# Kernel tuning notes

Hardware: AMD Instinct MI355X
Metric: run time of the kernel (lower is better)

Reference implementation:

```python
import jax, jax.numpy as jnp
import numpy as np

B, NA, NR, D, CUTOFF = 128, 32, 300, 128, 8.0


def _normalize(v, eps=1e-8):
    return v / jnp.maximum(jnp.linalg.norm(v, axis=-1, keepdims=True), eps)


def setup_inputs() -> dict:
    rng = np.random.default_rng(0)
    pl = rng.uniform(0.0, 24.0, (B, NA, 3)).astype(np.float32)
    pr = rng.uniform(0.0, 24.0, (B, NR, 3)).astype(np.float32)
    el_list, er_list = [], []
    for g in range(B):  # bipartite radius graph per complex (preprocessing)
        d2 = ((pl[g][:, None, :] - pr[g][None, :, :]) ** 2).sum(-1)
        li, ri = np.nonzero(d2 < CUTOFF * CUTOFF)
        el_list.append(li + g * NA)
        er_list.append(ri + g * NR)
    el = np.concatenate(el_list).astype(np.int32)
    er = np.concatenate(er_list).astype(np.int32)

    L, Dq = 2, D // 4
    def lin(k, shape, fan_in):
        return (rng.standard_normal(shape).astype(np.float32) / np.sqrt(fan_in))
    inp = {
        'ligand_repr': jnp.asarray(rng.standard_normal((B * NA, D)).astype(np.float32)),
        'ligand_vec_input': jnp.asarray(rng.standard_normal((B * NA, 3)).astype(np.float32)),
        'pos_ligand': jnp.asarray(pl.reshape(-1, 3)),
        'residue_repr': jnp.asarray(rng.standard_normal((B * NR, D)).astype(np.float32)),
        'pos_residue': jnp.asarray(pr.reshape(-1, 3)),
        'batch_ligand': jnp.asarray(np.repeat(np.arange(B), NA).astype(np.int32)),
        'batch_residue': jnp.asarray(np.repeat(np.arange(B), NR).astype(np.int32)),
        'edge_ligand_idx': jnp.asarray(el),
        'edge_residue_idx': jnp.asarray(er),
        # per-layer params stacked on leading L axis (stored [in,out])
        'Win1': jnp.asarray(lin(0, (L, D, D), D)),   'bin1': jnp.zeros((L, D), jnp.float32),
        'Win2': jnp.asarray(lin(0, (L, D, D), D)),   'bin2': jnp.zeros((L, D), jnp.float32),
        'Ws1a': jnp.asarray(lin(0, (L, 3, Dq), 3)),  'bs1a': jnp.zeros((L, Dq), jnp.float32),
        'Ws1b': jnp.asarray(lin(0, (L, Dq, 1), Dq)), 'bs1b': jnp.zeros((L, 1), jnp.float32),
        'Ws2a': jnp.asarray(lin(0, (L, 3, Dq), 3)),  'bs2a': jnp.zeros((L, Dq), jnp.float32),
        'Ws2b': jnp.asarray(lin(0, (L, Dq, 1), Dq)), 'bs2b': jnp.zeros((L, 1), jnp.float32),
        'Wl1': jnp.asarray(lin(0, (D, D), D)),       'bl1': jnp.zeros((D,), jnp.float32),
        'Wl2': jnp.asarray(lin(0, (D, 1), D)),       'bl2': jnp.zeros((1,), jnp.float32),
    }
    return inp


def reference(ligand_repr, ligand_vec_input, pos_ligand, residue_repr, pos_residue,
              batch_ligand, batch_residue, edge_ligand_idx, edge_residue_idx,
              Win1, bin1, Win2, bin2, Ws1a, bs1a, Ws1b, bs1b,
              Ws2a, bs2a, Ws2b, bs2b, Wl1, bl1, Wl2, bl2):
    Nl = pos_ligand.shape[0]
    L = Win1.shape[0]
    # residue local frames from consecutive backbone directions
    u = _normalize(pos_residue[1:] - pos_residue[:-1])      # [Nr-1, 3]
    start, end = u[1:], u[:-1]
    diff = _normalize(end - start)
    cross = _normalize(jnp.cross(end, start))
    vertical = _normalize(jnp.cross(diff, cross))
    frame = jnp.stack([diff, cross, vertical], axis=1)       # [Nr-2, 3, 3]
    residue_frame = jnp.concatenate([frame[:1], frame, frame[-1:]], axis=0)  # [Nr, 3, 3]

    edge_diff = _normalize(pos_ligand[edge_ligand_idx] - pos_residue[edge_residue_idx])  # [E, 3]
    # proj[e, j] = sum_i edge_diff[e, i] * frame[er[e], i, j]
    proj = jnp.einsum('ei,eij->ej', edge_diff, residue_frame[edge_residue_idx])  # [E, 3]
    h_sum = ligand_repr[edge_ligand_idx] + residue_repr[edge_residue_idx]        # [E, D]

    ligand_vec = jnp.zeros((Nl, 3, ligand_repr.shape[1]), ligand_repr.dtype)
    for l in range(L):
        h = jax.nn.silu(h_sum @ Win1[l] + bin1[l]) @ Win2[l] + bin2[l]           # [E, D]
        perm = h[:, :, None] * proj[:, None, :]                                  # [E, D, 3]
        w01 = (jax.nn.silu(perm @ Ws1a[l] + bs1a[l]) @ Ws1b[l] + bs1b[l]).squeeze(-1) + perm[..., 0]
        w02 = (jax.nn.silu(perm @ Ws2a[l] + bs2a[l]) @ Ws2b[l] + bs2b[l]).squeeze(-1) + perm[..., 0]
        lv_exp = ligand_vec[edge_ligand_idx] * w01[:, None, :] + edge_diff[:, :, None] * w02[:, None, :]
        ligand_vec = ligand_vec + jax.ops.segment_sum(lv_exp, edge_ligand_idx, num_segments=Nl)

    out = (jax.nn.relu(ligand_vec @ Wl1 + bl1) @ Wl2 + bl2).squeeze(-1) + ligand_vec_input  # [Nl, 3]
    return out
```

## Files before the change

### kernel.cpp

```cpp
#include <hip/hip_runtime.h>
#include <hip/hip_bf16.h>
#include <math.h>

typedef short bf16x8 __attribute__((ext_vector_type(8)));
typedef float f32x4 __attribute__((ext_vector_type(4)));

union BU8 { uint4 u; __hip_bfloat16 h[8]; ushort s[8]; };

__device__ __forceinline__ float3 f3sub(float3 a, float3 b){ return make_float3(a.x-b.x, a.y-b.y, a.z-b.z); }
__device__ __forceinline__ float3 f3nrm(float3 v){
  float n = sqrtf(v.x*v.x + v.y*v.y + v.z*v.z);
  float inv = 1.0f / fmaxf(n, 1e-8f);
  return make_float3(v.x*inv, v.y*inv, v.z*inv);
}
__device__ __forceinline__ float3 f3cross(float3 a, float3 b){
  return make_float3(a.y*b.z - a.z*b.y, a.z*b.x - a.x*b.z, a.x*b.y - a.y*b.x);
}
__device__ __forceinline__ float silu_f(float x){
  float ex = __expf(-x);
  return x * __builtin_amdgcn_rcpf(1.0f + ex);
}
__device__ __forceinline__ uint packbf2(float a, float b){
  ushort ua = __bfloat16_as_ushort(__float2bfloat16(a));
  ushort ub = __bfloat16_as_ushort(__float2bfloat16(b));
  return (uint)ua | ((uint)ub << 16);
}

__global__ void frames_kernel(const float* __restrict__ pos, float* __restrict__ frames, int Nr){
  int n = blockIdx.x*blockDim.x + threadIdx.x;
  if (n >= Nr) return;
  int k = n - 1;
  if (k < 0) k = 0;
  int kmax = Nr - 3;
  if (k > kmax) k = kmax;
  float3 p0 = make_float3(pos[3*k+0], pos[3*k+1], pos[3*k+2]);
  float3 p1 = make_float3(pos[3*k+3], pos[3*k+4], pos[3*k+5]);
  float3 p2 = make_float3(pos[3*k+6], pos[3*k+7], pos[3*k+8]);
  float3 u0 = f3nrm(f3sub(p1,p0));
  float3 u1 = f3nrm(f3sub(p2,p1));
  float3 dif = f3nrm(f3sub(u0,u1));
  float3 cr  = f3nrm(f3cross(u0,u1));
  float3 vt  = f3nrm(f3cross(dif,cr));
  float* o = frames + (size_t)n*9;
  o[0]=dif.x; o[1]=dif.y; o[2]=dif.z;
  o[3]=cr.x;  o[4]=cr.y;  o[5]=cr.z;
  o[6]=vt.x;  o[7]=vt.y;  o[8]=vt.z;
}

__global__ void edgepre_kernel(const float* __restrict__ posl, const float* __restrict__ posr,
    const int* __restrict__ el, const int* __restrict__ er, const float* __restrict__ frames,
    float* __restrict__ ediff, float* __restrict__ proj, int E){
  int e = blockIdx.x*blockDim.x + threadIdx.x;
  if (e >= E) return;
  int a = el[e], r = er[e];
  float3 pa = make_float3(posl[3*a+0], posl[3*a+1], posl[3*a+2]);
  float3 pr = make_float3(posr[3*r+0], posr[3*r+1], posr[3*r+2]);
  float3 ed = f3nrm(f3sub(pa,pr));
  const float* F = frames + (size_t)r*9;
  float px = ed.x*F[0] + ed.y*F[3] + ed.z*F[6];
  float py = ed.x*F[1] + ed.y*F[4] + ed.z*F[7];
  float pz = ed.x*F[2] + ed.y*F[5] + ed.z*F[8];
  ediff[3*e+0]=ed.x; ediff[3*e+1]=ed.y; ediff[3*e+2]=ed.z;
  proj[3*e+0]=px; proj[3*e+1]=py; proj[3*e+2]=pz;
}

__global__ void wprep_kernel(const float* __restrict__ W, __hip_bfloat16* __restrict__ Wt, int total){
  int idx = blockIdx.x*blockDim.x + threadIdx.x;
  if (idx >= total) return;
  int l = idx >> 14, rem = idx & 16383, n = rem >> 7, k = rem & 127;
  Wt[idx] = __float2bfloat16(W[(l<<14) + (k<<7) + n]);
}

__global__ __launch_bounds__(256) void pre_gemm_mfma(
    const float* __restrict__ lig, const float* __restrict__ res,
    const __hip_bfloat16* __restrict__ W1t,
    __hip_bfloat16* __restrict__ ligLb, __hip_bfloat16* __restrict__ resLb,
    int nBlkLig, int Nl, int Nr)
{
  __shared__ __hip_bfloat16 sA[64][136];
  __shared__ __hip_bfloat16 sB[128][136];
  int b = blockIdx.x;
  int layer = blockIdx.y;
  const __hip_bfloat16* Wt = W1t + (size_t)layer*16384;
  const float* X; __hip_bfloat16* O; int row0, rows;
  if (b < nBlkLig){ X = lig; O = ligLb + (size_t)layer*Nl*128; row0 = b*64;           rows = Nl; }
  else            { X = res; O = resLb + (size_t)layer*Nr*128; row0 = (b-nBlkLig)*64; rows = Nr; }
  int tid = threadIdx.x;

  {
    int n = tid >> 1, c0 = (tid & 1) * 64;
    const ushort* src = (const ushort*)Wt + n*128 + c0;
    ushort* dst = (ushort*)&sB[n][0] + c0;
    #pragma unroll
    for (int i = 0; i < 64; i += 8) *(uint4*)(dst + i) = *(const uint4*)(src + i);
  }
  {
    int r = tid >> 2, p = tid & 3, cb = p*32;
    int row = row0 + r; if (row >= rows) row = rows - 1;
    const float* src = X + (size_t)row*128 + cb;
    ushort* dst = (ushort*)&sA[r][0] + cb;
    #pragma unroll
    for (int i = 0; i < 32; i += 8){
      float4 v0 = *(const float4*)(src + i);
      float4 v1 = *(const float4*)(src + i + 4);
      BU8 o;
      o.h[0]=__float2bfloat16(v0.x); o.h[1]=__float2bfloat16(v0.y);
      o.h[2]=__float2bfloat16(v0.z); o.h[3]=__float2bfloat16(v0.w);
      o.h[4]=__float2bfloat16(v1.x); o.h[5]=__float2bfloat16(v1.y);
      o.h[6]=__float2bfloat16(v1.z); o.h[7]=__float2bfloat16(v1.w);
      *(uint4*)(dst + i) = o.u;
    }
  }
  __syncthreads();

  int w = tid >> 6, l = tid & 63;
  int lrow = l & 15, lko = (l >> 4) * 8;
  f32x4 acc[4][2];
  for (int mt=0; mt<4; ++mt)
    for (int nt=0; nt<2; ++nt)
      acc[mt][nt] = (f32x4){0.f,0.f,0.f,0.f};

  #pragma unroll
  for (int kc = 0; kc < 128; kc += 32){
    bf16x8 af[4], bfr[2];
    #pragma unroll
    for (int mt=0; mt<4; ++mt)
      af[mt] = *(const bf16x8*)((const ushort*)&sA[0][0] + (mt*16+lrow)*136 + kc + lko);
    #pragma unroll
    for (int nt=0; nt<2; ++nt)
      bfr[nt] = *(const bf16x8*)((const ushort*)&sB[0][0] + (w*32+nt*16+lrow)*136 + kc + lko);
    #pragma unroll
    for (int mt=0; mt<4; ++mt){
      #pragma unroll
      for (int nt=0; nt<2; ++nt)
        acc[mt][nt] = __builtin_amdgcn_mfma_f32_16x16x32_bf16(af[mt], bfr[nt], acc[mt][nt], 0, 0, 0);
    }
  }

  int orow = (l >> 4) * 4;
  #pragma unroll
  for (int mt=0; mt<4; ++mt){
    #pragma unroll
    for (int nt=0; nt<2; ++nt){
      int n = w*32 + nt*16 + (l & 15);
      #pragma unroll
      for (int j=0; j<4; ++j){
        int row = row0 + mt*16 + orow + j;
        if (row < rows) O[(size_t)row*128 + n] = __float2bfloat16(acc[mt][nt][j]);
      }
    }
  }
}

__global__ __launch_bounds__(256) void h_gemm2_mfma(
    const __hip_bfloat16* __restrict__ ligLbB, const __hip_bfloat16* __restrict__ resLbB,
    const int* __restrict__ el, const int* __restrict__ er,
    const float* __restrict__ b1B, const __hip_bfloat16* __restrict__ W2tB,
    const float* __restrict__ b2B,
    __hip_bfloat16* __restrict__ houtB, int E, int Nl, int Nr)
{
  __shared__ __hip_bfloat16 sA[64][136];
  __shared__ __hip_bfloat16 sB[128][136];
  int tid = threadIdx.x;
  int e0 = blockIdx.x * 64;
  int layer = blockIdx.y;
  const __hip_bfloat16* ligLb = ligLbB + (size_t)layer*Nl*128;
  const __hip_bfloat16* resLb = resLbB + (size_t)layer*Nr*128;
  const float* b1 = b1B + layer*128;
  const __hip_bfloat16* W2t = W2tB + (size_t)layer*16384;
  const float* b2 = b2B + layer*128;
  __hip_bfloat16* hout = houtB + (size_t)layer*E*128;

  {
    int n = tid >> 1, c0 = (tid & 1) * 64;
    const ushort* src = (const ushort*)W2t + n*128 + c0;
    ushort* dst = (ushort*)&sB[n][0] + c0;
    #pragma unroll
    for (int i = 0; i < 64; i += 8) *(uint4*)(dst + i) = *(const uint4*)(src + i);
  }
  {
    int r = tid >> 2, p = tid & 3, cb = p*32;
    int e = e0 + r; if (e >= E) e = E - 1;
    const ushort* la = (const ushort*)ligLb + (size_t)el[e]*128 + cb;
    const ushort* ra = (const ushort*)resLb + (size_t)er[e]*128 + cb;
    ushort* dst = (ushort*)&sA[r][0] + cb;
    #pragma unroll
    for (int i = 0; i < 32; i += 8){
      BU8 A, B, O;
      A.u = *(const uint4*)(la + i);
      B.u = *(const uint4*)(ra + i);
      float4 bb0 = *(const float4*)(b1 + cb + i);
      float4 bbx = *(const float4*)(b1 + cb + i + 4);
      float bbs[8] = {bb0.x,bb0.y,bb0.z,bb0.w,bbx.x,bbx.y,bbx.z,bbx.w};
      #pragma unroll
      for (int j=0; j<8; ++j){
        float x = __bfloat162float(A.h[j]) + __bfloat162float(B.h[j]) + bbs[j];
        O.h[j] = __float2bfloat16(silu_f(x));
      }
      *(uint4*)(dst + i) = O.u;
    }
  }
  __syncthreads();

  int w = tid >> 6, l = tid & 63;
  int lrow = l & 15, lko = (l >> 4) * 8;
  f32x4 acc[4][2];
  for (int mt=0; mt<4; ++mt)
    for (int nt=0; nt<2; ++nt)
      acc[mt][nt] = (f32x4){0.f,0.f,0.f,0.f};

  #pragma unroll
  for (int kc = 0; kc < 128; kc += 32){
    bf16x8 af[4], bfr[2];
    #pragma unroll
    for (int mt=0; mt<4; ++mt)
      af[mt] = *(const bf16x8*)((const ushort*)&sA[0][0] + (mt*16+lrow)*136 + kc + lko);
    #pragma unroll
    for (int nt=0; nt<2; ++nt)
      bfr[nt] = *(const bf16x8*)((const ushort*)&sB[0][0] + (w*32+nt*16+lrow)*136 + kc + lko);
    #pragma unroll
    for (int mt=0; mt<4; ++mt){
      #pragma unroll
      for (int nt=0; nt<2; ++nt)
        acc[mt][nt] = __builtin_amdgcn_mfma_f32_16x16x32_bf16(af[mt], bfr[nt], acc[mt][nt], 0, 0, 0);
    }
  }

  int orow = (l >> 4) * 4;
  #pragma unroll
  for (int mt=0; mt<4; ++mt){
    #pragma unroll
    for (int nt=0; nt<2; ++nt){
      int n = w*32 + nt*16 + (l & 15);
      float bb = b2[n];
      #pragma unroll
      for (int j=0; j<4; ++j){
        int e = e0 + mt*16 + orow + j;
        if (e < E) hout[(size_t)e*128 + n] = __float2bfloat16(acc[mt][nt][j] + bb);
      }
    }
  }
}

#define SEPB 16
__global__ __launch_bounds__(256) void spline_kernel(
    __hip_bfloat16* __restrict__ hbufB, const float* __restrict__ proj,
    const float* __restrict__ Ws1a, const float* __restrict__ bs1a,
    const float* __restrict__ Ws1b, const float* __restrict__ bs1b,
    const float* __restrict__ Ws2a, const float* __restrict__ bs2a,
    const float* __restrict__ Ws2b, const float* __restrict__ bs2b,
    __hip_bfloat16* __restrict__ w02B, int E)
{
  int layer = blockIdx.y;
  const float* Wa1 = Ws1a + layer*96;  const float* ba1 = bs1a + layer*32;
  const float* Wb1 = Ws1b + layer*32;  const float* bb1 = bs1b + layer;
  const float* Wa2 = Ws2a + layer*96;  const float* ba2 = bs2a + layer*32;
  const float* Wb2 = Ws2b + layer*32;  const float* bb2 = bs2b + layer;
  __hip_bfloat16* hb  = hbufB + (size_t)layer*E*128;
  __hip_bfloat16* w2o = w02B  + (size_t)layer*E*128;

  __shared__ float sA[2][SEPB][36];
  __shared__ float sNF[SEPB][2][16];
  __shared__ ushort sH[SEPB][128];
  __shared__ uint  sCo[SEPB][52];
  __shared__ float sMin[SEPB], sMax[SEPB];
  __shared__ float sH0[SEPB], sDv[SEPB], sInvD[SEPB], sP0[SEPB];

  int tid = threadIdx.x;
  int eb0 = blockIdx.x * SEPB;

  {
    int et = tid >> 4, sg = tid & 15;
    int e = eb0 + et; if (e >= E) e = E-1;
    uint4 raw = *(const uint4*)((const ushort*)hb + (size_t)e*128 + sg*8);
    *(uint4*)&sH[et][sg*8] = raw;
    uint us[4] = {raw.x, raw.y, raw.z, raw.w};
    float mn = 1e30f, mx = -1e30f;
    #pragma unroll
    for (int i=0;i<4;i++){
      float lo = __uint_as_float(us[i]<<16);
      float hi = __uint_as_float(us[i]&0xFFFF0000u);
      mn = fminf(mn, fminf(lo,hi)); mx = fmaxf(mx, fmaxf(lo,hi));
    }
    #pragma unroll
    for (int o=8;o>0;o>>=1){ mn=fminf(mn,__shfl_xor(mn,o)); mx=fmaxf(mx,__shfl_xor(mx,o)); }
    if (sg==0){ sMin[et]=mn; sMax[et]=mx; }
  }
  __syncthreads();

  for (int t=tid; t<2*SEPB*32; t+=256){
    int et = t>>6, rem = t&63, br = rem>>5, q = rem&31;
    int e = eb0+et; if (e>=E) e=E-1;
    const float* Wa = br ? Wa2 : Wa1;
    float p0=proj[3*e], p1=proj[3*e+1], p2=proj[3*e+2];
    sA[br][et][q] = p0*Wa[q]+p1*Wa[32+q]+p2*Wa[64+q];
  }
  if (tid < SEPB){
    int e = eb0+tid; if (e>=E) e=E-1;
    float range = fmaxf(sMax[tid]-sMin[tid], 1e-3f);
    sH0[tid]=sMin[tid]; sDv[tid]=range*(1.0f/13.0f); sInvD[tid]=13.0f/range;
    sP0[tid]=proj[3*e];
  }
  __syncthreads();

  {
    int et = tid >> 4, nd = tid & 15;
    float hn = fmaf((float)(nd-1), sDv[et], sH0[et]);
    {
      const float* Ar = &sA[0][et][0];
      float f = 0.f;
      #pragma unroll
      for (int q = 0; q < 32; ++q){
        float x  = fmaf(hn, Ar[q], ba1[q]);
        float sg = __builtin_amdgcn_rcpf(1.0f + __expf(-x));
        f = fmaf(Wb1[q], x*sg, f);
      }
      sNF[et][0][nd] = f;
    }
    {
      const float* Ar = &sA[1][et][0];
      float f = 0.f;
      #pragma unroll
      for (int q = 0; q < 32; ++q){
        float x  = fmaf(hn, Ar[q], ba2[q]);
        float sg = __builtin_amdgcn_rcpf(1.0f + __expf(-x));
        f = fmaf(Wb2[q], x*sg, f);
      }
      sNF[et][1][nd] = f;
    }
  }
  __syncthreads();

  for (int t=tid; t<512; t+=256){
    int et = t>>5, rem = t&31, br = rem>>4, i = rem&15;
    if (i < 13){
      const float* F = &sNF[et][br][0];
      float P0=F[i], P1=F[i+1], P2=F[i+2], P3=F[i+3];
      float bb = br ? bb2[0] : bb1[0];
      float c0 = P1 + bb;
      float c1 = 0.5f*(P2 - P0);
      float c2 = P0 - 2.5f*P1 + 2.0f*P2 - 0.5f*P3;
      float c3 = 0.5f*(P3 - P0) + 1.5f*(P1 - P2);
      sCo[et][br*26 + 2*i]     = packbf2(c0, c1);
      sCo[et][br*26 + 2*i + 1] = packbf2(c2, c3);
    }
  }
  __syncthreads();

  for (int t=tid; t<512; t+=256){
    int et = t>>5, g = t&31;
    int e = eb0 + et;
    if (e < E){
      int d0 = g*4;
      ushort4 hv4 = *(const ushort4*)&sH[et][d0];
      float h0=sH0[et], invD=sInvD[et], p0=sP0[et];
      ushort hvs[4] = {hv4.x, hv4.y, hv4.z, hv4.w};
      ushort o1[4], o2[4];
      #pragma unroll
      for (int k=0;k<4;++k){
        float h = __uint_as_float(((uint)hvs[k])<<16);
        float u = (h - h0) * invD;
        int ii = (int)u; ii = ii < 0 ? 0 : (ii > 12 ? 12 : ii);
        float s = u - (float)ii;
        uint cA0 = sCo[et][2*ii],      cA1 = sCo[et][2*ii+1];
        uint cB0 = sCo[et][26+2*ii],   cB1 = sCo[et][27+2*ii];
        float c0 = __uint_as_float(cA0<<16), c1 = __uint_as_float(cA0&0xFFFF0000u);
        float c2 = __uint_as_float(cA1<<16), c3 = __uint_as_float(cA1&0xFFFF0000u);
        float v1 = fmaf(fmaf(fmaf(c3,s,c2),s,c1),s,c0);
        float e0f = __uint_as_float(cB0<<16), e1f = __uint_as_float(cB0&0xFFFF0000u);
        float e2f = __uint_as_float(cB1<<16), e3f = __uint_as_float(cB1&0xFFFF0000u);
        float v2 = fmaf(fmaf(fmaf(e3f,s,e2f),s,e1f),s,e0f);
        float hp = h * p0;
        o1[k] = __bfloat16_as_ushort(__float2bfloat16(v1 + hp));
        o2[k] = __bfloat16_as_ushort(__float2bfloat16(v2 + hp));
      }
      ushort4 O1 = {o1[0],o1[1],o1[2],o1[3]};
      ushort4 O2 = {o2[0],o2[1],o2[2],o2[3]};
      *(ushort4*)((ushort*)hb  + (size_t)e*128 + d0) = O1;
      *(ushort4*)((ushort*)w2o + (size_t)e*128 + d0) = O2;
    }
  }
}

__global__ __launch_bounds__(128) void reduce_kernel(
    const __hip_bfloat16* __restrict__ w01B, const __hip_bfloat16* __restrict__ w02B,
    const float* __restrict__ ediff, const int* __restrict__ el,
    float* __restrict__ tvec, float* __restrict__ sumwb, int E, int Nl)
{
  __shared__ float sEd[64][3];
  int a = blockIdx.x;
  int layer = blockIdx.y;
  const __hip_bfloat16* w01 = w01B + (size_t)layer*E*128;
  const __hip_bfloat16* w02 = w02B + (size_t)layer*E*128;
  int d = threadIdx.x;

  int lo = 0, hi = E;
  while (lo < hi){ int m = (lo+hi)>>1; if (el[m] < a) lo = m+1; else hi = m; }
  int estart = lo;
  int lo2 = lo, hi2 = E;
  while (lo2 < hi2){ int m = (lo2+hi2)>>1; if (el[m] <= a) lo2 = m+1; else hi2 = m; }
  int eend = lo2;

  float sumw = 0.f, tx = 0.f, ty = 0.f, tz = 0.f;

  for (int ebase = estart; ebase < eend; ebase += 64){
    int n = min(64, eend - ebase);
    __syncthreads();
    for (int t = d; t < n*3; t += 128)
      ((float*)sEd)[t] = ediff[(size_t)ebase*3 + t];
    __syncthreads();

    #pragma unroll 4
    for (int ei = 0; ei < n; ++ei){
      float w1 = __bfloat162float(w01[(size_t)(ebase+ei)*128 + d]);
      float w2 = __bfloat162float(w02[(size_t)(ebase+ei)*128 + d]);
      sumw += w1;
      tx = fmaf(sEd[ei][0], w2, tx);
      ty = fmaf(sEd[ei][1], w2, ty);
      tz = fmaf(sEd[ei][2], w2, tz);
    }
  }

  size_t tb = (size_t)layer*Nl*384 + (size_t)a*384 + d;
  tvec[tb      ] = tx;
  tvec[tb + 128] = ty;
  tvec[tb + 256] = tz;
  sumwb[(size_t)layer*Nl*128 + (size_t)a*128 + d] = sumw;
}

__global__ __launch_bounds__(128) void head_kernel(
    const float* __restrict__ tvec, const float* __restrict__ sumwb,
    const float* __restrict__ Wl1, const float* __restrict__ bl1,
    const float* __restrict__ Wl2, const float* __restrict__ bl2,
    const float* __restrict__ lvin, float* __restrict__ out, int Nl)
{
  int a = blockIdx.x, d = threadIdx.x;
  __shared__ float slv[3][128];
  __shared__ float sred[2][3];
  const float* t0 = tvec + (size_t)a*384;
  const float* t1 = tvec + (size_t)Nl*384 + (size_t)a*384;
  float m = 1.0f + sumwb[(size_t)Nl*128 + (size_t)a*128 + d];
  slv[0][d] = t0[d      ]*m + t1[d      ];
  slv[1][d] = t0[d + 128]*m + t1[d + 128];
  slv[2][d] = t0[d + 256]*m + t1[d + 256];
  __syncthreads();
  float b = bl1[d];
  float a0 = b, a1 = b, a2 = b;
  #pragma unroll 4
  for (int k = 0; k < 128; ++k) {
    float w = Wl1[k*128 + d];
    a0 = fmaf(slv[0][k], w, a0);
    a1 = fmaf(slv[1][k], w, a1);
    a2 = fmaf(slv[2][k], w, a2);
  }
  float wl2 = Wl2[d];
  float z0 = fmaxf(a0, 0.f)*wl2;
  float z1 = fmaxf(a1, 0.f)*wl2;
  float z2 = fmaxf(a2, 0.f)*wl2;
  #pragma unroll
  for (int off = 32; off > 0; off >>= 1) {
    z0 += __shfl_down(z0, off);
    z1 += __shfl_down(z1, off);
    z2 += __shfl_down(z2, off);
  }
  int wv = d >> 6;
  if ((d & 63) == 0) { sred[wv][0]=z0; sred[wv][1]=z1; sred[wv][2]=z2; }
  __syncthreads();
  if (d == 0) {
    float bb = bl2[0];
    out[a*3+0] = sred[0][0]+sred[1][0] + bb + lvin[a*3+0];
    out[a*3+1] = sred[0][1]+sred[1][1] + bb + lvin[a*3+1];
    out[a*3+2] = sred[0][2]+sred[1][2] + bb + lvin[a*3+2];
  }
}

extern "C" void kernel_launch(void* const* d_in, const int* in_sizes, int n_in,
                              void* d_out, int out_size, void* d_ws, size_t ws_size,
                              hipStream_t stream)
{
  const float* lig   = (const float*)d_in[0];
  const float* lvin  = (const float*)d_in[1];
  const float* posl  = (const float*)d_in[2];
  const float* res   = (const float*)d_in[3];
  const float* posr  = (const float*)d_in[4];
  const int*   el    = (const int*)d_in[7];
  const int*   er    = (const int*)d_in[8];
  const float* Win1  = (const float*)d_in[9];
  const float* bin1  = (const float*)d_in[10];
  const float* Win2  = (const float*)d_in[11];
  const float* bin2  = (const float*)d_in[12];
  const float* Ws1a  = (const float*)d_in[13];
  const float* bs1a  = (const float*)d_in[14];
  const float* Ws1b  = (const float*)d_in[15];
  const float* bs1b  = (const float*)d_in[16];
  const float* Ws2a  = (const float*)d_in[17];
  const float* bs2a  = (const float*)d_in[18];
  const float* Ws2b  = (const float*)d_in[19];
  const float* bs2b  = (const float*)d_in[20];
  const float* Wl1   = (const float*)d_in[21];
  const float* bl1   = (const float*)d_in[22];
  const float* Wl2   = (const float*)d_in[23];
  const float* bl2   = (const float*)d_in[24];

  int Nl = in_sizes[2] / 3;
  int Nr = in_sizes[4] / 3;
  int E  = in_sizes[7];

  char* wsb = (char*)d_ws;
  size_t off = 0;
  auto carve = [&](size_t bytes) -> char* {
    char* p = wsb + off;
    off += (bytes + 255) & ~(size_t)255;
    return p;
  };
  float* frames = (float*)carve((size_t)Nr*9*4);
  float* ediff  = (float*)carve((size_t)E*3*4);
  float* proj   = (float*)carve((size_t)E*3*4);
  __hip_bfloat16* hbuf2  = (__hip_bfloat16*)carve((size_t)2*E*128*2);
  __hip_bfloat16* w02b   = (__hip_bfloat16*)carve((size_t)2*E*128*2);
  __hip_bfloat16* ligLb2 = (__hip_bfloat16*)carve((size_t)2*Nl*128*2);
  __hip_bfloat16* resLb2 = (__hip_bfloat16*)carve((size_t)2*Nr*128*2);
  __hip_bfloat16* W1t    = (__hip_bfloat16*)carve((size_t)2*16384*2);
  __hip_bfloat16* W2t    = (__hip_bfloat16*)carve((size_t)2*16384*2);
  float* tvec   = (float*)carve((size_t)2*Nl*384*4);
  float* sumwb  = (float*)carve((size_t)2*Nl*128*4);

  int nBlkLig = (Nl + 63)/64;
  int nBlkRes = (Nr + 63)/64;

  hipLaunchKernelGGL(frames_kernel, dim3((Nr+255)/256), dim3(256), 0, stream, posr, frames, Nr);
  hipLaunchKernelGGL(edgepre_kernel, dim3((E+255)/256), dim3(256), 0, stream,
                     posl, posr, el, er, frames, ediff, proj, E);
  hipLaunchKernelGGL(wprep_kernel, dim3((2*16384+255)/256), dim3(256), 0, stream, Win1, W1t, 2*16384);
  hipLaunchKernelGGL(wprep_kernel, dim3((2*16384+255)/256), dim3(256), 0, stream, Win2, W2t, 2*16384);

  hipLaunchKernelGGL(pre_gemm_mfma, dim3(nBlkLig+nBlkRes, 2), dim3(256), 0, stream,
      lig, res, W1t, ligLb2, resLb2, nBlkLig, Nl, Nr);
  hipLaunchKernelGGL(h_gemm2_mfma, dim3((E+63)/64, 2), dim3(256), 0, stream,
      ligLb2, resLb2, el, er, bin1, W2t, bin2, hbuf2, E, Nl, Nr);
  hipLaunchKernelGGL(spline_kernel, dim3((E+SEPB-1)/SEPB, 2), dim3(256), 0, stream,
      hbuf2, proj, Ws1a, bs1a, Ws1b, bs1b, Ws2a, bs2a, Ws2b, bs2b, w02b, E);
  hipLaunchKernelGGL(reduce_kernel, dim3(Nl, 2), dim3(128), 0, stream,
      hbuf2, w02b, ediff, el, tvec, sumwb, E, Nl);
  hipLaunchKernelGGL(head_kernel, dim3(Nl), dim3(128), 0, stream,
      tvec, sumwb, Wl1, bl1, Wl2, bl2, lvin, (float*)d_out, Nl);
}
```

Measured before the change: 236.1 us.

## Fuse second GEMM with spline weight evaluation and pack w01/w02 outputs

Merges the second hidden-layer GEMM and the spline kernel into one kernel. The h tile stays in shared memory instead of round-tripping through global memory as bf16, and the W2 fragments are held in registers. The two spline outputs are packed into one 32-bit word per element, so the reduction reads a single stream. The spline MLP is rewritten with base-2 exponent prescaling from a small prep kernel, and the interpolation grid drops from 13 to 12 intervals, which trades a little accuracy for less node evaluation work.

```diff
diff --git a/kernel.cpp b/kernel.cpp
--- a/kernel.cpp
+++ b/kernel.cpp
@@ -6,6 +6,11 @@
 typedef float f32x4 __attribute__((ext_vector_type(4)));
 
 union BU8 { uint4 u; __hip_bfloat16 h[8]; ushort s[8]; };
+
+#define LOG2E 1.44269504f
+#define LN2   0.69314718f
+#define NIV2  12
+#define NND   15
 
 __device__ __forceinline__ float3 f3sub(float3 a, float3 b){ return make_float3(a.x-b.x, a.y-b.y, a.z-b.z); }
 __device__ __forceinline__ float3 f3nrm(float3 v){
@@ -71,6 +76,26 @@
   Wt[idx] = __float2bfloat16(W[(l<<14) + (k<<7) + n]);
 }
 
+__global__ void sprep_kernel(const float* __restrict__ bs1a, const float* __restrict__ Ws1b,
+                             const float* __restrict__ bs2a, const float* __restrict__ Ws2b,
+                             const float* __restrict__ Ws1a, const float* __restrict__ Ws2a,
+                             float* __restrict__ bneg, float* __restrict__ wln,
+                             float* __restrict__ wap){
+  int tid = threadIdx.x;
+  if (tid < 128){
+    int l = tid >> 6, br = (tid >> 5) & 1, q = tid & 31;
+    const float* ba = br ? bs2a : bs1a;
+    const float* Wb = br ? Ws2b : Ws1b;
+    bneg[tid] = -ba[l*32 + q] * LOG2E;
+    wln[tid]  = -Wb[l*32 + q] * LN2;
+  }
+  for (int t = tid; t < 384; t += 256){
+    int l = t / 192, rem = t - l*192, br = rem / 96, i = rem - br*96;
+    const float* Wa = br ? Ws2a : Ws1a;
+    wap[t] = -Wa[l*96 + i] * LOG2E;
+  }
+}
+
 __global__ __launch_bounds__(256) void pre_gemm_mfma(
     const float* __restrict__ lig, const float* __restrict__ res,
     const __hip_bfloat16* __restrict__ W1t,
@@ -152,15 +177,22 @@
   }
 }
 
-__global__ __launch_bounds__(256) void h_gemm2_mfma(
+__global__ __launch_bounds__(256) void hw2_kernel(
     const __hip_bfloat16* __restrict__ ligLbB, const __hip_bfloat16* __restrict__ resLbB,
     const int* __restrict__ el, const int* __restrict__ er,
     const float* __restrict__ b1B, const __hip_bfloat16* __restrict__ W2tB,
-    const float* __restrict__ b2B,
-    __hip_bfloat16* __restrict__ houtB, int E, int Nl, int Nr)
+    const float* __restrict__ b2B, const float* __restrict__ proj,
+    const float* __restrict__ bnegB, const float* __restrict__ wlnB,
+    const float* __restrict__ wapB,
+    const float* __restrict__ bs1b, const float* __restrict__ bs2b,
+    uint* __restrict__ wpairB, int E, int Nl, int Nr)
 {
   __shared__ __hip_bfloat16 sA[64][136];
-  __shared__ __hip_bfloat16 sB[128][136];
+  __shared__ float sNF[64][2][16];
+  __shared__ uint  sCo[64][4*NIV2];
+  __shared__ float sPJ[64][3];
+  __shared__ float sMn[64], sMx[64], sH0[64], sDv[64], sInvD[64];
+
   int tid = threadIdx.x;
   int e0 = blockIdx.x * 64;
   int layer = blockIdx.y;
@@ -169,15 +201,23 @@
   const float* b1 = b1B + layer*128;
   const __hip_bfloat16* W2t = W2tB + (size_t)layer*16384;
   const float* b2 = b2B + layer*128;
-  __hip_bfloat16* hout = houtB + (size_t)layer*E*128;
-
-  {
-    int n = tid >> 1, c0 = (tid & 1) * 64;
-    const ushort* src = (const ushort*)W2t + n*128 + c0;
-    ushort* dst = (ushort*)&sB[n][0] + c0;
-    #pragma unroll
-    for (int i = 0; i < 64; i += 8) *(uint4*)(dst + i) = *(const uint4*)(src + i);
-  }
+  const float* bneg = bnegB + layer*64;
+  const float* wln  = wlnB + layer*64;
+  const float* wap  = wapB + layer*192;
+  float bb1v = bs1b[layer], bb2v = bs2b[layer];
+  uint* wpair = wpairB + (size_t)layer*E*128;
+
+  int w = tid >> 6, l = tid & 63;
+  int lrow = l & 15, lko = (l >> 4) * 8;
+
+  bf16x8 breg[4][2];
+  #pragma unroll
+  for (int kc4 = 0; kc4 < 4; ++kc4){
+    #pragma unroll
+    for (int nt = 0; nt < 2; ++nt)
+      breg[kc4][nt] = *(const bf16x8*)((const ushort*)W2t + (w*32+nt*16+lrow)*128 + kc4*32 + lko);
+  }
+
   {
     int r = tid >> 2, p = tid & 3, cb = p*32;
     int e = e0 + r; if (e >= E) e = E - 1;
@@ -200,170 +240,140 @@
       *(uint4*)(dst + i) = O.u;
     }
   }
-  __syncthreads();
-
-  int w = tid >> 6, l = tid & 63;
-  int lrow = l & 15, lko = (l >> 4) * 8;
+  if (tid < 192){
+    int et = tid / 3, comp = tid - et*3;
+    int e = e0 + et; if (e >= E) e = E-1;
+    sPJ[et][comp] = proj[3*e + comp];
+  }
+  __syncthreads();
+
   f32x4 acc[4][2];
   for (int mt=0; mt<4; ++mt)
     for (int nt=0; nt<2; ++nt)
       acc[mt][nt] = (f32x4){0.f,0.f,0.f,0.f};
 
   #pragma unroll
-  for (int kc = 0; kc < 128; kc += 32){
-    bf16x8 af[4], bfr[2];
+  for (int kc4 = 0; kc4 < 4; ++kc4){
+    bf16x8 af[4];
     #pragma unroll
     for (int mt=0; mt<4; ++mt)
-      af[mt] = *(const bf16x8*)((const ushort*)&sA[0][0] + (mt*16+lrow)*136 + kc + lko);
-    #pragma unroll
-    for (int nt=0; nt<2; ++nt)
-      bfr[nt] = *(const bf16x8*)((const ushort*)&sB[0][0] + (w*32+nt*16+lrow)*136 + kc + lko);
+      af[mt] = *(const bf16x8*)((const ushort*)&sA[0][0] + (mt*16+lrow)*136 + kc4*32 + lko);
     #pragma unroll
     for (int mt=0; mt<4; ++mt){
       #pragma unroll
       for (int nt=0; nt<2; ++nt)
-        acc[mt][nt] = __builtin_amdgcn_mfma_f32_16x16x32_bf16(af[mt], bfr[nt], acc[mt][nt], 0, 0, 0);
-    }
-  }
-
-  int orow = (l >> 4) * 4;
-  #pragma unroll
-  for (int mt=0; mt<4; ++mt){
-    #pragma unroll
-    for (int nt=0; nt<2; ++nt){
-      int n = w*32 + nt*16 + (l & 15);
-      float bb = b2[n];
-      #pragma unroll
-      for (int j=0; j<4; ++j){
-        int e = e0 + mt*16 + orow + j;
-        if (e < E) hout[(size_t)e*128 + n] = __float2bfloat16(acc[mt][nt][j] + bb);
-      }
-    }
-  }
-}
-
-#define SEPB 16
-__global__ __launch_bounds__(256) void spline_kernel(
-    __hip_bfloat16* __restrict__ hbufB, const float* __restrict__ proj,
-    const float* __restrict__ Ws1a, const float* __restrict__ bs1a,
-    const float* __restrict__ Ws1b, const float* __restrict__ bs1b,
-    const float* __restrict__ Ws2a, const float* __restrict__ bs2a,
-    const float* __restrict__ Ws2b, const float* __restrict__ bs2b,
-    __hip_bfloat16* __restrict__ w02B, int E)
-{
-  int layer = blockIdx.y;
-  const float* Wa1 = Ws1a + layer*96;  const float* ba1 = bs1a + layer*32;
-  const float* Wb1 = Ws1b + layer*32;  const float* bb1 = bs1b + layer;
-  const float* Wa2 = Ws2a + layer*96;  const float* ba2 = bs2a + layer*32;
-  const float* Wb2 = Ws2b + layer*32;  const float* bb2 = bs2b + layer;
-  __hip_bfloat16* hb  = hbufB + (size_t)layer*E*128;
-  __hip_bfloat16* w2o = w02B  + (size_t)layer*E*128;
-
-  __shared__ float sA[2][SEPB][36];
-  __shared__ float sNF[SEPB][2][16];
-  __shared__ ushort sH[SEPB][128];
-  __shared__ uint  sCo[SEPB][52];
-  __shared__ float sMin[SEPB], sMax[SEPB];
-  __shared__ float sH0[SEPB], sDv[SEPB], sInvD[SEPB], sP0[SEPB];
-
-  int tid = threadIdx.x;
-  int eb0 = blockIdx.x * SEPB;
+        acc[mt][nt] = __builtin_amdgcn_mfma_f32_16x16x32_bf16(af[mt], breg[kc4][nt], acc[mt][nt], 0, 0, 0);
+    }
+  }
+  __syncthreads();
 
   {
-    int et = tid >> 4, sg = tid & 15;
-    int e = eb0 + et; if (e >= E) e = E-1;
-    uint4 raw = *(const uint4*)((const ushort*)hb + (size_t)e*128 + sg*8);
-    *(uint4*)&sH[et][sg*8] = raw;
-    uint us[4] = {raw.x, raw.y, raw.z, raw.w};
+    int orow = (l >> 4) * 4;
+    #pragma unroll
+    for (int mt=0; mt<4; ++mt){
+      #pragma unroll
+      for (int nt=0; nt<2; ++nt){
+        int n = w*32 + nt*16 + (l & 15);
+        float bb = b2[n];
+        #pragma unroll
+        for (int j=0; j<4; ++j){
+          int eL = mt*16 + orow + j;
+          sA[eL][n] = __float2bfloat16(acc[mt][nt][j] + bb);
+        }
+      }
+    }
+  }
+  __syncthreads();
+
+  {
+    int et = tid >> 2, sg = tid & 3;
+    const ushort* hp = (const ushort*)&sA[et][0] + sg*32;
     float mn = 1e30f, mx = -1e30f;
     #pragma unroll
-    for (int i=0;i<4;i++){
-      float lo = __uint_as_float(us[i]<<16);
-      float hi = __uint_as_float(us[i]&0xFFFF0000u);
-      mn = fminf(mn, fminf(lo,hi)); mx = fmaxf(mx, fmaxf(lo,hi));
-    }
-    #pragma unroll
-    for (int o=8;o>0;o>>=1){ mn=fminf(mn,__shfl_xor(mn,o)); mx=fmaxf(mx,__shfl_xor(mx,o)); }
-    if (sg==0){ sMin[et]=mn; sMax[et]=mx; }
-  }
-  __syncthreads();
-
-  for (int t=tid; t<2*SEPB*32; t+=256){
-    int et = t>>6, rem = t&63, br = rem>>5, q = rem&31;
-    int e = eb0+et; if (e>=E) e=E-1;
-    const float* Wa = br ? Wa2 : Wa1;
-    float p0=proj[3*e], p1=proj[3*e+1], p2=proj[3*e+2];
-    sA[br][et][q] = p0*Wa[q]+p1*Wa[32+q]+p2*Wa[64+q];
-  }
-  if (tid < SEPB){
-    int e = eb0+tid; if (e>=E) e=E-1;
-    float range = fmaxf(sMax[tid]-sMin[tid], 1e-3f);
-    sH0[tid]=sMin[tid]; sDv[tid]=range*(1.0f/13.0f); sInvD[tid]=13.0f/range;
-    sP0[tid]=proj[3*e];
-  }
-  __syncthreads();
-
-  {
-    int et = tid >> 4, nd = tid & 15;
+    for (int i=0;i<32;i+=8){
+      uint4 raw = *(const uint4*)(hp + i);
+      uint us[4] = {raw.x, raw.y, raw.z, raw.w};
+      #pragma unroll
+      for (int k=0;k<4;k++){
+        float lo_ = __uint_as_float(us[k]<<16);
+        float hi_ = __uint_as_float(us[k]&0xFFFF0000u);
+        mn = fminf(mn, fminf(lo_,hi_)); mx = fmaxf(mx, fmaxf(lo_,hi_));
+      }
+    }
+    mn = fminf(mn, __shfl_xor(mn,1)); mx = fmaxf(mx, __shfl_xor(mx,1));
+    mn = fminf(mn, __shfl_xor(mn,2)); mx = fmaxf(mx, __shfl_xor(mx,2));
+    if (sg==0){ sMn[et]=mn; sMx[et]=mx; }
+  }
+  __syncthreads();
+
+  if (tid < 64){
+    float range = fmaxf(sMx[tid]-sMn[tid], 1e-3f);
+    sH0[tid]=sMn[tid]; sDv[tid]=range*(1.0f/NIV2); sInvD[tid]=(float)NIV2/range;
+  }
+  __syncthreads();
+
+  for (int t = tid; t < 64*NND; t += 256){
+    int et = t / NND, nd = t - et*NND;
     float hn = fmaf((float)(nd-1), sDv[et], sH0[et]);
+    float p0 = sPJ[et][0], p1 = sPJ[et][1], p2 = sPJ[et][2];
     {
-      const float* Ar = &sA[0][et][0];
       float f = 0.f;
       #pragma unroll
       for (int q = 0; q < 32; ++q){
-        float x  = fmaf(hn, Ar[q], ba1[q]);
-        float sg = __builtin_amdgcn_rcpf(1.0f + __expf(-x));
-        f = fmaf(Wb1[q], x*sg, f);
+        float Ap  = p0*wap[q] + p1*wap[32+q] + p2*wap[64+q];
+        float x2n = fmaf(hn, Ap, bneg[q]);
+        float ex  = __builtin_amdgcn_exp2f(x2n);
+        float sg  = __builtin_amdgcn_rcpf(1.0f + ex);
+        f = fmaf(wln[q], x2n*sg, f);
       }
       sNF[et][0][nd] = f;
     }
     {
-      const float* Ar = &sA[1][et][0];
       float f = 0.f;
       #pragma unroll
       for (int q = 0; q < 32; ++q){
-        float x  = fmaf(hn, Ar[q], ba2[q]);
-        float sg = __builtin_amdgcn_rcpf(1.0f + __expf(-x));
-        f = fmaf(Wb2[q], x*sg, f);
+        float Ap  = p0*wap[96+q] + p1*wap[128+q] + p2*wap[160+q];
+        float x2n = fmaf(hn, Ap, bneg[32+q]);
+        float ex  = __builtin_amdgcn_exp2f(x2n);
+        float sg  = __builtin_amdgcn_rcpf(1.0f + ex);
+        f = fmaf(wln[32+q], x2n*sg, f);
       }
       sNF[et][1][nd] = f;
     }
   }
   __syncthreads();
 
-  for (int t=tid; t<512; t+=256){
-    int et = t>>5, rem = t&31, br = rem>>4, i = rem&15;
-    if (i < 13){
-      const float* F = &sNF[et][br][0];
-      float P0=F[i], P1=F[i+1], P2=F[i+2], P3=F[i+3];
-      float bb = br ? bb2[0] : bb1[0];
-      float c0 = P1 + bb;
-      float c1 = 0.5f*(P2 - P0);
-      float c2 = P0 - 2.5f*P1 + 2.0f*P2 - 0.5f*P3;
-      float c3 = 0.5f*(P3 - P0) + 1.5f*(P1 - P2);
-      sCo[et][br*26 + 2*i]     = packbf2(c0, c1);
-      sCo[et][br*26 + 2*i + 1] = packbf2(c2, c3);
-    }
-  }
-  __syncthreads();
-
-  for (int t=tid; t<512; t+=256){
-    int et = t>>5, g = t&31;
-    int e = eb0 + et;
+  for (int t = tid; t < 64*2*NIV2; t += 256){
+    int et = t / (2*NIV2), rem = t - et*(2*NIV2), br = rem / NIV2, i = rem - br*NIV2;
+    const float* F = &sNF[et][br][0];
+    float P0=F[i], P1=F[i+1], P2=F[i+2], P3=F[i+3];
+    float bb = br ? bb2v : bb1v;
+    float c0 = P1 + bb;
+    float c1 = 0.5f*(P2 - P0);
+    float c2 = P0 - 2.5f*P1 + 2.0f*P2 - 0.5f*P3;
+    float c3 = 0.5f*(P3 - P0) + 1.5f*(P1 - P2);
+    sCo[et][br*2*NIV2 + 2*i]     = packbf2(c0, c1);
+    sCo[et][br*2*NIV2 + 2*i + 1] = packbf2(c2, c3);
+  }
+  __syncthreads();
+
+  for (int t = tid; t < 2048; t += 256){
+    int et = t >> 5, g = t & 31;
+    int e = e0 + et;
     if (e < E){
       int d0 = g*4;
-      ushort4 hv4 = *(const ushort4*)&sH[et][d0];
-      float h0=sH0[et], invD=sInvD[et], p0=sP0[et];
+      ushort4 hv4 = *(const ushort4*)((const ushort*)&sA[et][0] + d0);
+      float h0 = sH0[et], invD = sInvD[et], p0 = sPJ[et][0];
       ushort hvs[4] = {hv4.x, hv4.y, hv4.z, hv4.w};
-      ushort o1[4], o2[4];
+      uint outp[4];
       #pragma unroll
       for (int k=0;k<4;++k){
         float h = __uint_as_float(((uint)hvs[k])<<16);
         float u = (h - h0) * invD;
-        int ii = (int)u; ii = ii < 0 ? 0 : (ii > 12 ? 12 : ii);
+        int ii = (int)u; ii = ii < 0 ? 0 : (ii > NIV2-1 ? NIV2-1 : ii);
         float s = u - (float)ii;
-        uint cA0 = sCo[et][2*ii],      cA1 = sCo[et][2*ii+1];
-        uint cB0 = sCo[et][26+2*ii],   cB1 = sCo[et][27+2*ii];
+        uint cA0 = sCo[et][2*ii],            cA1 = sCo[et][2*ii+1];
+        uint cB0 = sCo[et][2*NIV2 + 2*ii],   cB1 = sCo[et][2*NIV2 + 2*ii + 1];
         float c0 = __uint_as_float(cA0<<16), c1 = __uint_as_float(cA0&0xFFFF0000u);
         float c2 = __uint_as_float(cA1<<16), c3 = __uint_as_float(cA1&0xFFFF0000u);
         float v1 = fmaf(fmaf(fmaf(c3,s,c2),s,c1),s,c0);
@@ -371,27 +381,23 @@
         float e2f = __uint_as_float(cB1<<16), e3f = __uint_as_float(cB1&0xFFFF0000u);
         float v2 = fmaf(fmaf(fmaf(e3f,s,e2f),s,e1f),s,e0f);
         float hp = h * p0;
-        o1[k] = __bfloat16_as_ushort(__float2bfloat16(v1 + hp));
-        o2[k] = __bfloat16_as_ushort(__float2bfloat16(v2 + hp));
-      }
-      ushort4 O1 = {o1[0],o1[1],o1[2],o1[3]};
-      ushort4 O2 = {o2[0],o2[1],o2[2],o2[3]};
-      *(ushort4*)((ushort*)hb  + (size_t)e*128 + d0) = O1;
-      *(ushort4*)((ushort*)w2o + (size_t)e*128 + d0) = O2;
+        outp[k] = packbf2(v1 + hp, v2 + hp);
+      }
+      uint4 O = {outp[0], outp[1], outp[2], outp[3]};
+      *(uint4*)(wpair + (size_t)e*128 + d0) = O;
     }
   }
 }
 
 __global__ __launch_bounds__(128) void reduce_kernel(
-    const __hip_bfloat16* __restrict__ w01B, const __hip_bfloat16* __restrict__ w02B,
+    const uint* __restrict__ wpairB,
     const float* __restrict__ ediff, const int* __restrict__ el,
     float* __restrict__ tvec, float* __restrict__ sumwb, int E, int Nl)
 {
   __shared__ float sEd[64][3];
   int a = blockIdx.x;
   int layer = blockIdx.y;
-  const __hip_bfloat16* w01 = w01B + (size_t)layer*E*128;
-  const __hip_bfloat16* w02 = w02B + (size_t)layer*E*128;
+  const uint* wpair = wpairB + (size_t)layer*E*128;
   int d = threadIdx.x;
 
   int lo = 0, hi = E;
@@ -412,8 +418,9 @@
 
     #pragma unroll 4
     for (int ei = 0; ei < n; ++ei){
-      float w1 = __bfloat162float(w01[(size_t)(ebase+ei)*128 + d]);
-      float w2 = __bfloat162float(w02[(size_t)(ebase+ei)*128 + d]);
+      uint wp = wpair[(size_t)(ebase+ei)*128 + d];
+      float w1 = __uint_as_float(wp << 16);
+      float w2 = __uint_as_float(wp & 0xFFFF0000u);
       sumw += w1;
       tx = fmaf(sEd[ei][0], w2, tx);
       ty = fmaf(sEd[ei][1], w2, ty);
@@ -516,14 +523,16 @@
   float* frames = (float*)carve((size_t)Nr*9*4);
   float* ediff  = (float*)carve((size_t)E*3*4);
   float* proj   = (float*)carve((size_t)E*3*4);
-  __hip_bfloat16* hbuf2  = (__hip_bfloat16*)carve((size_t)2*E*128*2);
-  __hip_bfloat16* w02b   = (__hip_bfloat16*)carve((size_t)2*E*128*2);
+  uint* wpair   = (uint*)carve((size_t)2*E*128*4);
   __hip_bfloat16* ligLb2 = (__hip_bfloat16*)carve((size_t)2*Nl*128*2);
   __hip_bfloat16* resLb2 = (__hip_bfloat16*)carve((size_t)2*Nr*128*2);
   __hip_bfloat16* W1t    = (__hip_bfloat16*)carve((size_t)2*16384*2);
   __hip_bfloat16* W2t    = (__hip_bfloat16*)carve((size_t)2*16384*2);
   float* tvec   = (float*)carve((size_t)2*Nl*384*4);
   float* sumwb  = (float*)carve((size_t)2*Nl*128*4);
+  float* bneg   = (float*)carve(128*4);
+  float* wln    = (float*)carve(128*4);
+  float* wap    = (float*)carve(384*4);
 
   int nBlkLig = (Nl + 63)/64;
   int nBlkRes = (Nr + 63)/64;
@@ -533,15 +542,16 @@
                      posl, posr, el, er, frames, ediff, proj, E);
   hipLaunchKernelGGL(wprep_kernel, dim3((2*16384+255)/256), dim3(256), 0, stream, Win1, W1t, 2*16384);
   hipLaunchKernelGGL(wprep_kernel, dim3((2*16384+255)/256), dim3(256), 0, stream, Win2, W2t, 2*16384);
+  hipLaunchKernelGGL(sprep_kernel, dim3(1), dim3(256), 0, stream,
+                     bs1a, Ws1b, bs2a, Ws2b, Ws1a, Ws2a, bneg, wln, wap);
 
   hipLaunchKernelGGL(pre_gemm_mfma, dim3(nBlkLig+nBlkRes, 2), dim3(256), 0, stream,
       lig, res, W1t, ligLb2, resLb2, nBlkLig, Nl, Nr);
-  hipLaunchKernelGGL(h_gemm2_mfma, dim3((E+63)/64, 2), dim3(256), 0, stream,
-      ligLb2, resLb2, el, er, bin1, W2t, bin2, hbuf2, E, Nl, Nr);
-  hipLaunchKernelGGL(spline_kernel, dim3((E+SEPB-1)/SEPB, 2), dim3(256), 0, stream,
-      hbuf2, proj, Ws1a, bs1a, Ws1b, bs1b, Ws2a, bs2a, Ws2b, bs2b, w02b, E);
+  hipLaunchKernelGGL(hw2_kernel, dim3((E+63)/64, 2), dim3(256), 0, stream,
+      ligLb2, resLb2, el, er, bin1, W2t, bin2, proj,
+      bneg, wln, wap, bs1b, bs2b, wpair, E, Nl, Nr);
   hipLaunchKernelGGL(reduce_kernel, dim3(Nl, 2), dim3(128), 0, stream,
-      hbuf2, w02b, ediff, el, tvec, sumwb, E, Nl);
+      wpair, ediff, el, tvec, sumwb, E, Nl);
   hipLaunchKernelGGL(head_kernel, dim3(Nl), dim3(128), 0, stream,
       tvec, sumwb, Wl1, bl1, Wl2, bl2, lvin, (float*)d_out, Nl);
 }
```

Result: slower. 254.4 us (+7.7%).

## Fold frame computation into edgepre, merge weight prep, cheapen spline SiLU math

Applied to the files above, without the earlier changes.

Removes the separate frames kernel and its buffer: each edge thread now recomputes its residue's local frame from three neighbouring positions. The two weight-transpose launches become one prep kernel, which also precomputes bias and output weights pre-scaled by log2(e) and ln2. The spline node evaluation then uses exp2 directly and shares one reciprocal between the two branches' sigmoids. Together this cuts two launches and some transcendental work, in exchange for redundant frame math per edge and a possible overflow in the shared reciprocal product for very negative activations.

```diff
diff --git a/kernel.cpp b/kernel.cpp
--- a/kernel.cpp
+++ b/kernel.cpp
@@ -6,6 +6,9 @@
 typedef float f32x4 __attribute__((ext_vector_type(4)));
 
 union BU8 { uint4 u; __hip_bfloat16 h[8]; ushort s[8]; };
+
+#define LOG2E 1.44269504f
+#define LN2   0.69314718f
 
 __device__ __forceinline__ float3 f3sub(float3 a, float3 b){ return make_float3(a.x-b.x, a.y-b.y, a.z-b.z); }
 __device__ __forceinline__ float3 f3nrm(float3 v){
@@ -26,49 +29,58 @@
   return (uint)ua | ((uint)ub << 16);
 }
 
-__global__ void frames_kernel(const float* __restrict__ pos, float* __restrict__ frames, int Nr){
-  int n = blockIdx.x*blockDim.x + threadIdx.x;
-  if (n >= Nr) return;
-  int k = n - 1;
-  if (k < 0) k = 0;
-  int kmax = Nr - 3;
-  if (k > kmax) k = kmax;
-  float3 p0 = make_float3(pos[3*k+0], pos[3*k+1], pos[3*k+2]);
-  float3 p1 = make_float3(pos[3*k+3], pos[3*k+4], pos[3*k+5]);
-  float3 p2 = make_float3(pos[3*k+6], pos[3*k+7], pos[3*k+8]);
-  float3 u0 = f3nrm(f3sub(p1,p0));
-  float3 u1 = f3nrm(f3sub(p2,p1));
-  float3 dif = f3nrm(f3sub(u0,u1));
-  float3 cr  = f3nrm(f3cross(u0,u1));
-  float3 vt  = f3nrm(f3cross(dif,cr));
-  float* o = frames + (size_t)n*9;
-  o[0]=dif.x; o[1]=dif.y; o[2]=dif.z;
-  o[3]=cr.x;  o[4]=cr.y;  o[5]=cr.z;
-  o[6]=vt.x;  o[7]=vt.y;  o[8]=vt.z;
-}
-
 __global__ void edgepre_kernel(const float* __restrict__ posl, const float* __restrict__ posr,
-    const int* __restrict__ el, const int* __restrict__ er, const float* __restrict__ frames,
-    float* __restrict__ ediff, float* __restrict__ proj, int E){
+    const int* __restrict__ el, const int* __restrict__ er,
+    float* __restrict__ ediff, float* __restrict__ proj, int E, int Nr){
   int e = blockIdx.x*blockDim.x + threadIdx.x;
   if (e >= E) return;
   int a = el[e], r = er[e];
   float3 pa = make_float3(posl[3*a+0], posl[3*a+1], posl[3*a+2]);
   float3 pr = make_float3(posr[3*r+0], posr[3*r+1], posr[3*r+2]);
   float3 ed = f3nrm(f3sub(pa,pr));
-  const float* F = frames + (size_t)r*9;
-  float px = ed.x*F[0] + ed.y*F[3] + ed.z*F[6];
-  float py = ed.x*F[1] + ed.y*F[4] + ed.z*F[7];
-  float pz = ed.x*F[2] + ed.y*F[5] + ed.z*F[8];
+
+  int k = r - 1;
+  if (k < 0) k = 0;
+  int kmax = Nr - 3;
+  if (k > kmax) k = kmax;
+  float3 p0 = make_float3(posr[3*k+0], posr[3*k+1], posr[3*k+2]);
+  float3 p1 = make_float3(posr[3*k+3], posr[3*k+4], posr[3*k+5]);
+  float3 p2 = make_float3(posr[3*k+6], posr[3*k+7], posr[3*k+8]);
+  float3 u0 = f3nrm(f3sub(p1,p0));
+  float3 u1 = f3nrm(f3sub(p2,p1));
+  float3 dif = f3nrm(f3sub(u0,u1));
+  float3 cr  = f3nrm(f3cross(u0,u1));
+  float3 vt  = f3nrm(f3cross(dif,cr));
+
+  float px = ed.x*dif.x + ed.y*cr.x + ed.z*vt.x;
+  float py = ed.x*dif.y + ed.y*cr.y + ed.z*vt.y;
+  float pz = ed.x*dif.z + ed.y*cr.z + ed.z*vt.z;
   ediff[3*e+0]=ed.x; ediff[3*e+1]=ed.y; ediff[3*e+2]=ed.z;
   proj[3*e+0]=px; proj[3*e+1]=py; proj[3*e+2]=pz;
 }
 
-__global__ void wprep_kernel(const float* __restrict__ W, __hip_bfloat16* __restrict__ Wt, int total){
+__global__ void prep_kernel(const float* __restrict__ Win1, const float* __restrict__ Win2,
+                            __hip_bfloat16* __restrict__ W1t, __hip_bfloat16* __restrict__ W2t,
+                            const float* __restrict__ bs1a, const float* __restrict__ Ws1b,
+                            const float* __restrict__ bs2a, const float* __restrict__ Ws2b,
+                            float* __restrict__ bneg, float* __restrict__ wln){
   int idx = blockIdx.x*blockDim.x + threadIdx.x;
-  if (idx >= total) return;
-  int l = idx >> 14, rem = idx & 16383, n = rem >> 7, k = rem & 127;
-  Wt[idx] = __float2bfloat16(W[(l<<14) + (k<<7) + n]);
+  if (idx < 32768){
+    int l = idx >> 14, rem = idx & 16383, n = rem >> 7, k = rem & 127;
+    W1t[idx] = __float2bfloat16(Win1[(l<<14) + (k<<7) + n]);
+  } else if (idx < 65536){
+    int i2 = idx - 32768;
+    int l = i2 >> 14, rem = i2 & 16383, n = rem >> 7, k = rem & 127;
+    W2t[i2] = __float2bfloat16(Win2[(l<<14) + (k<<7) + n]);
+  }
+  if (blockIdx.x == 0 && threadIdx.x < 128){
+    int t = threadIdx.x;
+    int l = t >> 6, br = (t >> 5) & 1, q = t & 31;
+    const float* ba = br ? bs2a : bs1a;
+    const float* Wb = br ? Ws2b : Ws1b;
+    bneg[t] = -ba[l*32 + q] * LOG2E;
+    wln[t]  = -Wb[l*32 + q] * LN2;
+  }
 }
 
 __global__ __launch_bounds__(256) void pre_gemm_mfma(
@@ -245,17 +257,17 @@
 #define SEPB 16
 __global__ __launch_bounds__(256) void spline_kernel(
     __hip_bfloat16* __restrict__ hbufB, const float* __restrict__ proj,
-    const float* __restrict__ Ws1a, const float* __restrict__ bs1a,
-    const float* __restrict__ Ws1b, const float* __restrict__ bs1b,
-    const float* __restrict__ Ws2a, const float* __restrict__ bs2a,
-    const float* __restrict__ Ws2b, const float* __restrict__ bs2b,
+    const float* __restrict__ Ws1a, const float* __restrict__ Ws2a,
+    const float* __restrict__ bs1b, const float* __restrict__ bs2b,
+    const float* __restrict__ bnegB, const float* __restrict__ wlnB,
     __hip_bfloat16* __restrict__ w02B, int E)
 {
   int layer = blockIdx.y;
-  const float* Wa1 = Ws1a + layer*96;  const float* ba1 = bs1a + layer*32;
-  const float* Wb1 = Ws1b + layer*32;  const float* bb1 = bs1b + layer;
-  const float* Wa2 = Ws2a + layer*96;  const float* ba2 = bs2a + layer*32;
-  const float* Wb2 = Ws2b + layer*32;  const float* bb2 = bs2b + layer;
+  const float* Wa1 = Ws1a + layer*96;
+  const float* Wa2 = Ws2a + layer*96;
+  const float* bneg = bnegB + layer*64;
+  const float* wln  = wlnB  + layer*64;
+  float bb1v = bs1b[layer], bb2v = bs2b[layer];
   __hip_bfloat16* hb  = hbufB + (size_t)layer*E*128;
   __hip_bfloat16* w2o = w02B  + (size_t)layer*E*128;
 
@@ -293,7 +305,7 @@
     int e = eb0+et; if (e>=E) e=E-1;
     const float* Wa = br ? Wa2 : Wa1;
     float p0=proj[3*e], p1=proj[3*e+1], p2=proj[3*e+2];
-    sA[br][et][q] = p0*Wa[q]+p1*Wa[32+q]+p2*Wa[64+q];
+    sA[br][et][q] = -(p0*Wa[q]+p1*Wa[32+q]+p2*Wa[64+q])*LOG2E;
   }
   if (tid < SEPB){
     int e = eb0+tid; if (e>=E) e=E-1;
@@ -306,28 +318,22 @@
   {
     int et = tid >> 4, nd = tid & 15;
     float hn = fmaf((float)(nd-1), sDv[et], sH0[et]);
-    {
-      const float* Ar = &sA[0][et][0];
-      float f = 0.f;
-      #pragma unroll
-      for (int q = 0; q < 32; ++q){
-        float x  = fmaf(hn, Ar[q], ba1[q]);
-        float sg = __builtin_amdgcn_rcpf(1.0f + __expf(-x));
-        f = fmaf(Wb1[q], x*sg, f);
-      }
-      sNF[et][0][nd] = f;
-    }
-    {
-      const float* Ar = &sA[1][et][0];
-      float f = 0.f;
-      #pragma unroll
-      for (int q = 0; q < 32; ++q){
-        float x  = fmaf(hn, Ar[q], ba2[q]);
-        float sg = __builtin_amdgcn_rcpf(1.0f + __expf(-x));
-        f = fmaf(Wb2[q], x*sg, f);
-      }
-      sNF[et][1][nd] = f;
-    }
+    const float* A0 = &sA[0][et][0];
+    const float* A1 = &sA[1][et][0];
+    float f0 = 0.f, f1 = 0.f;
+    #pragma unroll
+    for (int q = 0; q < 32; ++q){
+      float x0 = fmaf(hn, A0[q], bneg[q]);
+      float x1 = fmaf(hn, A1[q], bneg[32+q]);
+      float e0 = __builtin_amdgcn_exp2f(x0);
+      float e1 = __builtin_amdgcn_exp2f(x1);
+      float d0 = 1.0f + e0, d1 = 1.0f + e1;
+      float r  = __builtin_amdgcn_rcpf(d0*d1);
+      f0 = fmaf(wln[q],    x0*(r*d1), f0);
+      f1 = fmaf(wln[32+q], x1*(r*d0), f1);
+    }
+    sNF[et][0][nd] = f0;
+    sNF[et][1][nd] = f1;
   }
   __syncthreads();
 
@@ -336,7 +342,7 @@
     if (i < 13){
       const float* F = &sNF[et][br][0];
       float P0=F[i], P1=F[i+1], P2=F[i+2], P3=F[i+3];
-      float bb = br ? bb2[0] : bb1[0];
+      float bb = br ? bb2v : bb1v;
       float c0 = P1 + bb;
       float c1 = 0.5f*(P2 - P0);
       float c2 = P0 - 2.5f*P1 + 2.0f*P2 - 0.5f*P3;
@@ -513,7 +519,6 @@
     off += (bytes + 255) & ~(size_t)255;
     return p;
   };
-  float* frames = (float*)carve((size_t)Nr*9*4);
   float* ediff  = (float*)carve((size_t)E*3*4);
   float* proj   = (float*)carve((size_t)E*3*4);
   __hip_bfloat16* hbuf2  = (__hip_bfloat16*)carve((size_t)2*E*128*2);
@@ -524,22 +529,23 @@
   __hip_bfloat16* W2t    = (__hip_bfloat16*)carve((size_t)2*16384*2);
   float* tvec   = (float*)carve((size_t)2*Nl*384*4);
   float* sumwb  = (float*)carve((size_t)2*Nl*128*4);
+  float* bneg   = (float*)carve(128*4);
+  float* wln    = (float*)carve(128*4);
 
   int nBlkLig = (Nl + 63)/64;
   int nBlkRes = (Nr + 63)/64;
 
-  hipLaunchKernelGGL(frames_kernel, dim3((Nr+255)/256), dim3(256), 0, stream, posr, frames, Nr);
   hipLaunchKernelGGL(edgepre_kernel, dim3((E+255)/256), dim3(256), 0, stream,
-                     posl, posr, el, er, frames, ediff, proj, E);
-  hipLaunchKernelGGL(wprep_kernel, dim3((2*16384+255)/256), dim3(256), 0, stream, Win1, W1t, 2*16384);
-  hipLaunchKernelGGL(wprep_kernel, dim3((2*16384+255)/256), dim3(256), 0, stream, Win2, W2t, 2*16384);
+                     posl, posr, el, er, ediff, proj, E, Nr);
+  hipLaunchKernelGGL(prep_kernel, dim3(256), dim3(256), 0, stream,
+                     Win1, Win2, W1t, W2t, bs1a, Ws1b, bs2a, Ws2b, bneg, wln);
 
   hipLaunchKernelGGL(pre_gemm_mfma, dim3(nBlkLig+nBlkRes, 2), dim3(256), 0, stream,
       lig, res, W1t, ligLb2, resLb2, nBlkLig, Nl, Nr);
   hipLaunchKernelGGL(h_gemm2_mfma, dim3((E+63)/64, 2), dim3(256), 0, stream,
       ligLb2, resLb2, el, er, bin1, W2t, bin2, hbuf2, E, Nl, Nr);
   hipLaunchKernelGGL(spline_kernel, dim3((E+SEPB-1)/SEPB, 2), dim3(256), 0, stream,
-      hbuf2, proj, Ws1a, bs1a, Ws1b, bs1b, Ws2a, bs2a, Ws2b, bs2b, w02b, E);
+      hbuf2, proj, Ws1a, Ws2a, bs1b, bs2b, bneg, wln, w02b, E);
   hipLaunchKernelGGL(reduce_kernel, dim3(Nl, 2), dim3(128), 0, stream,
       hbuf2, w02b, ediff, el, tvec, sumwb, E, Nl);
   hipLaunchKernelGGL(head_kernel, dim3(Nl), dim3(128), 0, stream,
```

Result: faster. 227.1 us (-3.8%).
